# Kernel optimization log

Hardware: AMD Instinct MI355X
Metric: run time of the kernel (lower is better)

The kernel has to match this reference:

```python
import jax, jax.numpy as jnp
import numpy as np


def haar_level(x):
    """One 2D Haar (periodization-equivalent for even sizes) DWT on [B,K,C,H,W].
    Returns [B,4K,C,H/2,W/2] with per-parent band order (LL, Hx, Hy, Hxy),
    matching the tree's append order yl, yh0, yh1, yh2."""
    B, K, C, H, W = x.shape
    x = x.reshape(B, K, C, H // 2, 2, W // 2, 2)
    a = x[:, :, :, :, 0, :, 0]
    b = x[:, :, :, :, 0, :, 1]
    c = x[:, :, :, :, 1, :, 0]
    d = x[:, :, :, :, 1, :, 1]
    ll = (a + b + c + d) * 0.5
    h1 = (a - b + c - d) * 0.5   # high along width
    h2 = (a + b - c - d) * 0.5   # high along height
    h3 = (a - b - c + d) * 0.5   # diagonal
    out = jnp.stack([ll, h1, h2, h3], axis=2)  # [B,K,4,C,H/2,W/2]
    return out.reshape(B, 4 * K, C, H // 2, W // 2)


def conv2d(x, w, b, stride, pad):
    y = jax.lax.conv_general_dilated(
        x, w, window_strides=(stride, stride),
        padding=[(pad, pad), (pad, pad)],
        dimension_numbers=('NCHW', 'OIHW', 'NCHW'))
    return y + b[None, :, None, None]


def setup_inputs() -> dict:
    key = jax.random.key(0)
    ks = jax.random.split(key, 9)
    s = 0.05
    return {
        'x':        jax.random.normal(ks[0], (64, 3, 224, 224), dtype=jnp.float32),
        'w_s1':     jax.random.normal(ks[1], (192, 3, 7, 7), dtype=jnp.float32) * s,
        'b_s1':     jax.random.normal(ks[2], (192,), dtype=jnp.float32) * s,
        'w_s2':     jax.random.normal(ks[3], (192, 192, 7, 7), dtype=jnp.float32) * s,
        'b_s2':     jax.random.normal(ks[4], (192,), dtype=jnp.float32) * s,
        'w_p':      jax.random.normal(ks[5], (768, 960, 3, 3), dtype=jnp.float32) * s,
        'b_p':      jax.random.normal(ks[6], (768,), dtype=jnp.float32) * s,
        'cls_token': jax.random.normal(ks[7], (1, 1, 768), dtype=jnp.float32),
        'positions': jax.random.normal(ks[8], (50, 768), dtype=jnp.float32),
    }


def reference(x, w_s1, b_s1, w_s2, b_s2, w_p, b_p, cls_token, positions):
    B = x.shape[0]
    # ---- 4-level full Haar wavelet packet tree (vectorized over subbands) ----
    t = x[:, None]                      # [B,1,3,224,224]
    for _ in range(4):
        t = haar_level(t)               # -> [B,256,3,14,14]
    wav = t.reshape(B, 256 * 3, 14, 14)  # [B,768,14,14] (tree concat order)
    # ---- spatial branch: two strided 7x7 convs (224 -> 56 -> 14) ----
    sp = conv2d(x, w_s1, b_s1, stride=4, pad=3)
    sp = conv2d(sp, w_s2, b_s2, stride=4, pad=3)   # [B,192,14,14]
    feat = jnp.concatenate([wav, sp], axis=1)      # [B,960,14,14]
    # ---- patch projection conv 3x3 s2 -> 7x7, flatten to tokens ----
    y = conv2d(feat, w_p, b_p, stride=2, pad=1)    # [B,768,7,7]
    y = y.reshape(B, 768, 49).transpose(0, 2, 1)   # [B,49,768]
    cls = jnp.broadcast_to(cls_token, (B, 1, 768))
    y = jnp.concatenate([cls, y], axis=1) + positions  # [B,50,768]
    return y
```

## Files before the change

### kernel.cpp

```cpp
#include <hip/hip_runtime.h>
#include <stdint.h>

typedef __attribute__((ext_vector_type(8))) short short8;
typedef __attribute__((ext_vector_type(4))) float floatx4;

__device__ inline unsigned short f2bf(float f){
  union { float fv; unsigned int u; } v; v.fv = f;
  unsigned int u = v.u;
  unsigned int r = ((u >> 16) & 1u) + 0x7FFFu;
  return (unsigned short)((u + r) >> 16);
}

__device__ __forceinline__ void async16(const void* g, void* l){
  __builtin_amdgcn_global_load_lds(
      (const __attribute__((address_space(1))) unsigned int*)g,
      (__attribute__((address_space(3))) unsigned int*)l, 16, 0, 0);
}

#define PBAR(N) do {                                              \
    asm volatile("s_waitcnt vmcnt(" #N ")" ::: "memory");          \
    __builtin_amdgcn_s_barrier();                                  \
    asm volatile("" ::: "memory");                                 \
  } while (0)

__global__ void prep_w1(const float* __restrict__ w, unsigned short* __restrict__ w1p){
  int i = blockIdx.x*256 + threadIdx.x;
  if (i >= 192*192) return;
  int k = i % 192, o = i / 192;
  int cc = k >> 3, kx = k & 7;
  unsigned short v = 0;
  if (cc < 21 && kx < 7){
    int c = cc / 7, ky = cc % 7;
    v = f2bf(w[(o*3 + c)*49 + ky*7 + kx]);
  }
  w1p[i] = v;
}
__global__ void prep_w2(const float* __restrict__ w, unsigned short* __restrict__ w2p){
  int i = blockIdx.x*256 + threadIdx.x;
  if (i >= 192*9408) return;
  int k = i % 9408, o = i / 9408;
  int g = k / 192, c = k % 192;
  int ky = g / 7, kx = g % 7;
  w2p[i] = f2bf(w[((o*192 + c)*7 + ky)*7 + kx]);
}
__global__ void prep_w3(const float* __restrict__ w, unsigned short* __restrict__ w3p){
  int i = blockIdx.x*256 + threadIdx.x;
  if (i >= 768*8640) return;
  int k = i % 8640, o = i / 8640;
  int g = k / 960, c = k % 960;
  int ky = g / 3, kx = g % 3;
  w3p[i] = f2bf(w[((o*960 + c)*3 + ky)*3 + kx]);
}
__global__ void prep_zp(unsigned int* __restrict__ zp){
  zp[threadIdx.x] = 0u;
}
__global__ void zero_f32(float* __restrict__ p, int n){
  int i = blockIdx.x*256 + threadIdx.x;
  if (i < n) p[i] = 0.f;
}

__global__ void pad_x2(const float* __restrict__ x, unsigned short* __restrict__ xh2){
  int idx = blockIdx.x*256 + threadIdx.x;
  if (idx >= 64*3*230*56*8) return;
  int kx = idx & 7; int t = idx >> 3;
  int ox = t % 56;  t /= 56;
  int iy = t % 230; t /= 230;
  int row = iy - 3;
  int col = 4*ox - 3 + kx;
  unsigned short v = 0;
  if (row >= 0 && row < 224 && col >= 0 && col < 224)
    v = f2bf(x[((size_t)t*224 + row)*224 + col]);
  xh2[idx] = v;
}

__global__ void wavelet_kernel(const float* __restrict__ x, unsigned short* __restrict__ feat){
  int blk = blockIdx.x;
  int j = blk % 14; blk /= 14;
  int i = blk % 14; blk /= 14;
  int c = blk % 3;  int b = blk / 3;
  int t = threadIdx.x;
  int u = t >> 4, v = t & 15;
  float val = x[((size_t)(b*3 + c)*224 + (i*16 + u))*224 + (j*16 + v)];
  #pragma unroll
  for (int bit = 1; bit < 64; bit <<= 1){
    float p = __shfl_xor(val, bit);
    val = (t & bit) ? (p - val) : (val + p);
  }
  __shared__ float s[256];
  #pragma unroll
  for (int bit = 64; bit < 256; bit <<= 1){
    s[t] = val; __syncthreads();
    float p = s[t ^ bit]; __syncthreads();
    val = (t & bit) ? (p - val) : (val + p);
  }
  s[t] = val; __syncthreads();
  int k = t;
  int d1 = (k>>6)&3, d2 = (k>>4)&3, d3 = (k>>2)&3, d4 = k&3;
  int mr = (d1>>1) | ((d2>>1)<<1) | ((d3>>1)<<2) | ((d4>>1)<<3);
  int mc = (d1&1)  | ((d2&1)<<1)  | ((d3&1)<<2)  | ((d4&1)<<3);
  float outv = s[mr*16 + mc] * 0.0625f;
  feat[((size_t)((b*14 + i)*14 + j))*960 + (k*3 + c)] = f2bf(outv);
}

__global__ __launch_bounds__(256) void conv1_gemm(const unsigned short* __restrict__ xh2,
                                                  const unsigned short* __restrict__ w1p,
                                                  const float* __restrict__ b1,
                                                  unsigned short* __restrict__ sp1){
  __shared__ unsigned short As[2][128*64], Bs[2][64*64];
  int m0 = blockIdx.x*128, n0 = blockIdx.y*64;
  int tid = threadIdx.x, wave = tid >> 6, lane = tid & 63;
  int l16 = lane & 15, quad = lane >> 4;
  int wy = wave >> 1, wx = wave & 1;
  int r8 = lane >> 3, kb = (lane & 7) ^ r8;

  int Abase[4];
  #pragma unroll
  for (int j = 0; j < 4; j++){
    int row = wave*32 + j*8 + r8;
    int m = m0 + row;
    int ox = m % 56; int t = m / 56; int oy = t % 56; int b = t / 56;
    Abase[j] = (b*690 + 4*oy)*448 + ox*8;
  }
  const unsigned short* pB0 = w1p + (n0 + wave*16 + r8)*192 + kb*8;
  const unsigned short* pB1 = pB0 + 8*192;

  int sw = l16 & 7;
  int xo0 = ((quad    ) ^ sw)*8;
  int xo1 = ((quad + 4) ^ sw)*8;
  int aoff[4];
  #pragma unroll
  for (int mt = 0; mt < 4; mt++) aoff[mt] = (wy*64 + mt*16 + l16)*64;
  int boff0 = (wx*32 + l16)*64, boff1 = boff0 + 16*64;

  floatx4 acc[4][2];
  #pragma unroll
  for (int mt = 0; mt < 4; mt++)
    #pragma unroll
    for (int nt = 0; nt < 2; nt++) acc[mt][nt] = (floatx4){0.f,0.f,0.f,0.f};

  auto stage = [&](int i, int buf){
    int cc = i*8 + kb;
    int c = (cc*147) >> 10;
    int ky = cc - 7*c;
    int koff = (c*230 + ky)*448;
    #pragma unroll
    for (int j = 0; j < 4; j++)
      async16(xh2 + Abase[j] + koff, (void*)&As[buf][(wave*32 + j*8)*64]);
    async16(pB0 + i*64, (void*)&Bs[buf][(wave*16    )*64]);
    async16(pB1 + i*64, (void*)&Bs[buf][(wave*16 + 8)*64]);
  };

  stage(0, 0);
  __syncthreads();
  #pragma unroll
  for (int i = 0; i < 3; i++){
    int buf = i & 1;
    if (i < 2) stage(i+1, buf ^ 1);
    #pragma unroll
    for (int ks = 0; ks < 2; ks++){
      int xo = ks ? xo1 : xo0;
      short8 b0 = *(const short8*)&Bs[buf][boff0 + xo];
      short8 b1 = *(const short8*)&Bs[buf][boff1 + xo];
      #pragma unroll
      for (int mt = 0; mt < 4; mt++){
        short8 a = *(const short8*)&As[buf][aoff[mt] + xo];
        acc[mt][0] = __builtin_amdgcn_mfma_f32_16x16x32_bf16(a, b0, acc[mt][0], 0, 0, 0);
        acc[mt][1] = __builtin_amdgcn_mfma_f32_16x16x32_bf16(a, b1, acc[mt][1], 0, 0, 0);
      }
    }
    __syncthreads();
  }

  #pragma unroll
  for (int mt = 0; mt < 4; mt++){
    #pragma unroll
    for (int rg = 0; rg < 4; rg++){
      int row = wy*64 + mt*16 + quad*4 + rg;
      size_t ob = (size_t)(m0 + row)*192;
      #pragma unroll
      for (int nt = 0; nt < 2; nt++){
        int nn = n0 + wx*32 + nt*16 + l16;
        sp1[ob + nn] = f2bf(acc[mt][nt][rg] + b1[nn]);
      }
    }
  }
}

template<int MODE>
__global__ __launch_bounds__(256, 4) void conv_ks(const unsigned short* __restrict__ Ain,
                                                  const unsigned short* __restrict__ Bt,
                                                  const unsigned short* __restrict__ zp,
                                                  float* __restrict__ pout){
  constexpr int OH  = (MODE==2) ? 14 : 7;
  constexpr int OW  = OH;
  constexpr int IH  = (MODE==2) ? 56 : 14;
  constexpr int IW  = IH;
  constexpr int Cin = (MODE==2) ? 192 : 960;
  constexpr int KW  = (MODE==2) ? 7 : 3;
  constexpr int S   = (MODE==2) ? 4 : 2;
  constexpr int P   = (MODE==2) ? 3 : 1;
  constexpr int K   = (MODE==2) ? 9408 : 8640;
  constexpr int K2  = K/2;
  constexpr int NB  = K2/32;
  constexpr int MTI = (MODE==2) ? 98 : 25;
  constexpr int NTI = (MODE==2) ? 3 : 12;
  constexpr int GRP = 8*NTI;
  constexpr int PERSEG = (MODE==2) ? 13*GRP : 4*GRP;
  constexpr int M   = (MODE==2) ? 12544 : 3136;
  constexpr int NF  = (MODE==2) ? 192 : 768;

  int id = blockIdx.x;
  int kseg = id / PERSEG; int rem = id % PERSEG;
  int g = rem / GRP, r2 = rem % GRP;
  int mtile = g*8 + (r2 & 7);
  if (mtile >= MTI) return;
  int ntile = r2 >> 3;
  int m0 = mtile*128, n0 = ntile*64;

  __shared__ unsigned short As[3][4096], Bs[3][2048];

  int tid = threadIdx.x, wv = tid >> 6, lane = tid & 63;
  int l16 = lane & 15, quad = lane >> 4;
  int wy = wv >> 1, wx = wv & 1;

  int rl = lane >> 2;
  int go = ((lane & 3) ^ ((lane >> 3) & 3))*8;

  int iyb[2], ixb[2], abase[2];
  #pragma unroll
  for (int j = 0; j < 2; j++){
    int r = (wv + j*4)*16 + rl;
    int m = m0 + r; if (MODE == 3 && m > M-1) m = M-1;
    int ox = m % OW; int t = m / OW; int oy = t % OH; int bb = t / OH;
    iyb[j] = S*oy - P; ixb[j] = S*ox - P;
    abase[j] = ((bb*IH + iyb[j])*IW + ixb[j])*Cin + go;
  }
  const unsigned short* pB = Bt + (size_t)(n0 + wv*16 + rl)*K + kseg*K2 + go;

  int k0 = kseg*K2;
  int c0 = k0 % Cin;
  int gk = k0 / Cin;
  int ky = gk / KW, kx = gk % KW;
  int k0n = 0;

  int xo = (quad ^ ((l16 >> 1) & 3))*8;

  floatx4 acc[4][2];
  #pragma unroll
  for (int mt = 0; mt < 4; mt++)
    #pragma unroll
    for (int nt = 0; nt < 2; nt++) acc[mt][nt] = (floatx4){0.f,0.f,0.f,0.f};

  auto stage = [&](int buf){
    int koff = (ky*IW + kx)*Cin + c0;
    #pragma unroll
    for (int j = 0; j < 2; j++){
      int iy = iyb[j] + ky, ix = ixb[j] + kx;
      const unsigned short* pa = ((unsigned)iy < (unsigned)IH && (unsigned)ix < (unsigned)IW)
                                 ? (Ain + abase[j] + koff) : zp;
      async16(pa, (void*)&As[buf][(wv + j*4)*512]);
    }
    async16(pB + k0n, (void*)&Bs[buf][wv*512]);
    k0n += 32;
    c0 += 32;
    if (c0 == Cin){ c0 = 0; kx++; if (kx == KW){ kx = 0; ky++; } }
  };

  auto compute = [&](int buf){
    short8 b0 = *(const short8*)&Bs[buf][(wx*32      + l16)*32 + xo];
    short8 b1 = *(const short8*)&Bs[buf][(wx*32 + 16 + l16)*32 + xo];
    short8 a0 = *(const short8*)&As[buf][(wy*64       + l16)*32 + xo];
    short8 a1 = *(const short8*)&As[buf][(wy*64 + 16  + l16)*32 + xo];
    short8 a2 = *(const short8*)&As[buf][(wy*64 + 32  + l16)*32 + xo];
    short8 a3 = *(const short8*)&As[buf][(wy*64 + 48  + l16)*32 + xo];
    acc[0][0] = __builtin_amdgcn_mfma_f32_16x16x32_bf16(a0, b0, acc[0][0], 0, 0, 0);
    acc[0][1] = __builtin_amdgcn_mfma_f32_16x16x32_bf16(a0, b1, acc[0][1], 0, 0, 0);
    acc[1][0] = __builtin_amdgcn_mfma_f32_16x16x32_bf16(a1, b0, acc[1][0], 0, 0, 0);
    acc[1][1] = __builtin_amdgcn_mfma_f32_16x16x32_bf16(a1, b1, acc[1][1], 0, 0, 0);
    acc[2][0] = __builtin_amdgcn_mfma_f32_16x16x32_bf16(a2, b0, acc[2][0], 0, 0, 0);
    acc[2][1] = __builtin_amdgcn_mfma_f32_16x16x32_bf16(a2, b1, acc[2][1], 0, 0, 0);
    acc[3][0] = __builtin_amdgcn_mfma_f32_16x16x32_bf16(a3, b0, acc[3][0], 0, 0, 0);
    acc[3][1] = __builtin_amdgcn_mfma_f32_16x16x32_bf16(a3, b1, acc[3][1], 0, 0, 0);
  };

  stage(0); stage(1);
  int bc = 0;
  for (int i = 0; i < NB - 2; i++){
    PBAR(3);
    int bn = bc + 2; if (bn >= 3) bn -= 3;
    stage(bn);
    compute(bc);
    bc = (bc == 2) ? 0 : bc + 1;
  }
  PBAR(3);
  compute(bc);
  bc = (bc == 2) ? 0 : bc + 1;
  PBAR(0);
  compute(bc);

  #pragma unroll
  for (int mt = 0; mt < 4; mt++){
    #pragma unroll
    for (int rg = 0; rg < 4; rg++){
      int row = wy*64 + mt*16 + quad*4 + rg;
      int mm = m0 + row;
      if (MODE == 3 && mm >= M) continue;
      #pragma unroll
      for (int nt = 0; nt < 2; nt++){
        int nn = n0 + wx*32 + nt*16 + l16;
        atomicAdd(&pout[(size_t)mm*NF + nn], acc[mt][nt][rg]);
      }
    }
  }
}

__global__ void comb2(const float* __restrict__ pc, const float* __restrict__ bias,
                      unsigned short* __restrict__ feat){
  int i = blockIdx.x*256 + threadIdx.x;
  int n = i % 192, m = i / 192;
  feat[(size_t)m*960 + 768 + n] = f2bf(pc[i] + bias[n]);
}
__global__ void comb3(const float* __restrict__ pc, const float* __restrict__ bias,
                      const float* __restrict__ pos, float* __restrict__ out){
  int i = blockIdx.x*256 + threadIdx.x;
  int n = i % 768, m = i / 768;
  int b2 = m / 49, tt = m - b2*49;
  float v = pc[(size_t)m*768 + n] + bias[n] + pos[(size_t)(1 + tt)*768 + n];
  out[((size_t)(m + b2 + 1))*768 + n] = v;
}

__global__ void cls_kernel(const float* __restrict__ cls, const float* __restrict__ pos,
                           float* __restrict__ out){
  int i = blockIdx.x*256 + threadIdx.x;
  if (i >= 64*768) return;
  int e = i % 768, b = i / 768;
  out[(size_t)(b*50)*768 + e] = cls[e] + pos[e];
}

extern "C" void kernel_launch(void* const* d_in, const int* in_sizes, int n_in,
                              void* d_out, int out_size, void* d_ws, size_t ws_size,
                              hipStream_t stream){
  (void)in_sizes; (void)n_in; (void)out_size;
  const float* x    = (const float*)d_in[0];
  const float* w_s1 = (const float*)d_in[1];
  const float* b_s1 = (const float*)d_in[2];
  const float* w_s2 = (const float*)d_in[3];
  const float* b_s2 = (const float*)d_in[4];
  const float* w_p  = (const float*)d_in[5];
  const float* b_p  = (const float*)d_in[6];
  const float* cls  = (const float*)d_in[7];
  const float* pos  = (const float*)d_in[8];
  float* out = (float*)d_out;

  char* ws = (char*)d_ws;
  if (ws_size < 118235136u) return;
  unsigned short* w1p  = (unsigned short*)(ws + 0);
  unsigned short* sp1  = (unsigned short*)(ws + 131072);
  unsigned short* zp   = (unsigned short*)(ws + 77201408u);
  unsigned short* w2p  = (unsigned short*)(ws + 77266944u);
  unsigned short* w3p  = (unsigned short*)(ws + 80879616u);
  unsigned short* feat = (unsigned short*)(ws + 94150656u);
  unsigned short* xh2  = (unsigned short*)(ws + 77266944u);
  float* pc2 = (float*)(ws + 80879616u);
  float* pc3 = (float*)(ws + 131072);

  prep_w1<<<(192*192 + 255)/256, 256, 0, stream>>>(w_s1, w1p);
  pad_x2<<<(64*3*230*56*8)/256, 256, 0, stream>>>(x, xh2);
  conv1_gemm<<<dim3(1568, 3), 256, 0, stream>>>(xh2, w1p, b_s1, sp1);
  prep_w2<<<(192*9408 + 255)/256, 256, 0, stream>>>(w_s2, w2p);
  prep_zp<<<1, 64, 0, stream>>>((unsigned int*)zp);
  wavelet_kernel<<<64*3*14*14, 256, 0, stream>>>(x, feat);

  zero_f32<<<9408, 256, 0, stream>>>(pc2, 12544*192);
  conv_ks<2><<<624, 256, 0, stream>>>(sp1, w2p, zp, pc2);
  comb2<<<9408, 256, 0, stream>>>(pc2, b_s2, feat);

  prep_w3<<<(768*8640 + 255)/256, 256, 0, stream>>>(w_p, w3p);
  zero_f32<<<9600, 256, 0, stream>>>(pc3, 3200*768);
  conv_ks<3><<<768, 256, 0, stream>>>(feat, w3p, zp, pc3);
  comb3<<<9408, 256, 0, stream>>>(pc3, b_p, pos, out);
  cls_kernel<<<(64*768 + 255)/256, 256, 0, stream>>>(cls, pos, out);
}
```

Baseline: 457.3 us.

## Split conv K-reduction into four segments and vectorize padded input staging

The split-K factor of both implicit-GEMM convolutions goes from 2 to 4, with segment bounds computed in 32-wide K blocks, and the grid sizes are doubled to match. The aim is to give the GPU more blocks, since 624 or 768 blocks leave it underfilled. The cost is more atomic or partial-sum traffic into the fp32 accumulators. Separately, the input padding kernel now has each thread build 8 bf16 values and write them with one 16-byte store, instead of one thread per element.

```diff
diff --git a/kernel.cpp b/kernel.cpp
--- a/kernel.cpp
+++ b/kernel.cpp
@@ -59,18 +59,22 @@
   if (i < n) p[i] = 0.f;
 }
 
-__global__ void pad_x2(const float* __restrict__ x, unsigned short* __restrict__ xh2){
+__global__ void pad_x8(const float* __restrict__ x, unsigned short* __restrict__ xh2){
   int idx = blockIdx.x*256 + threadIdx.x;
-  if (idx >= 64*3*230*56*8) return;
-  int kx = idx & 7; int t = idx >> 3;
-  int ox = t % 56;  t /= 56;
-  int iy = t % 230; t /= 230;
+  int ox = idx % 56; int t = idx / 56;
+  int iy = t % 230;  t /= 230;
   int row = iy - 3;
-  int col = 4*ox - 3 + kx;
-  unsigned short v = 0;
-  if (row >= 0 && row < 224 && col >= 0 && col < 224)
-    v = f2bf(x[((size_t)t*224 + row)*224 + col]);
-  xh2[idx] = v;
+  short8 o = (short8){0,0,0,0,0,0,0,0};
+  if ((unsigned)row < 224u){
+    const float* src = x + ((size_t)t*224 + row)*224;
+    int cbase = 4*ox - 3;
+    #pragma unroll
+    for (int kx = 0; kx < 8; kx++){
+      int col = cbase + kx;
+      if ((unsigned)col < 224u) o[kx] = (short)f2bf(src[col]);
+    }
+  }
+  *(short8*)(xh2 + (size_t)idx*8) = o;
 }
 
 __global__ void wavelet_kernel(const float* __restrict__ x, unsigned short* __restrict__ feat){
@@ -200,8 +204,8 @@
   constexpr int S   = (MODE==2) ? 4 : 2;
   constexpr int P   = (MODE==2) ? 3 : 1;
   constexpr int K   = (MODE==2) ? 9408 : 8640;
-  constexpr int K2  = K/2;
-  constexpr int NB  = K2/32;
+  constexpr int NBODY = K/32;
+  constexpr int KSEG  = 4;
   constexpr int MTI = (MODE==2) ? 98 : 25;
   constexpr int NTI = (MODE==2) ? 3 : 12;
   constexpr int GRP = 8*NTI;
@@ -217,6 +221,10 @@
   int ntile = r2 >> 3;
   int m0 = mtile*128, n0 = ntile*64;
 
+  int bs = (NBODY*kseg)/KSEG, be = (NBODY*(kseg+1))/KSEG;
+  int NB = be - bs;
+  int k0 = bs*32;
+
   __shared__ unsigned short As[3][4096], Bs[3][2048];
 
   int tid = threadIdx.x, wv = tid >> 6, lane = tid & 63;
@@ -235,9 +243,8 @@
     iyb[j] = S*oy - P; ixb[j] = S*ox - P;
     abase[j] = ((bb*IH + iyb[j])*IW + ixb[j])*Cin + go;
   }
-  const unsigned short* pB = Bt + (size_t)(n0 + wv*16 + rl)*K + kseg*K2 + go;
-
-  int k0 = kseg*K2;
+  const unsigned short* pB = Bt + (size_t)(n0 + wv*16 + rl)*K + k0 + go;
+
   int c0 = k0 % Cin;
   int gk = k0 / Cin;
   int ky = gk / KW, kx = gk % KW;
@@ -365,19 +372,19 @@
   float* pc3 = (float*)(ws + 131072);
 
   prep_w1<<<(192*192 + 255)/256, 256, 0, stream>>>(w_s1, w1p);
-  pad_x2<<<(64*3*230*56*8)/256, 256, 0, stream>>>(x, xh2);
+  pad_x8<<<64*3*230*56/256, 256, 0, stream>>>(x, xh2);
   conv1_gemm<<<dim3(1568, 3), 256, 0, stream>>>(xh2, w1p, b_s1, sp1);
   prep_w2<<<(192*9408 + 255)/256, 256, 0, stream>>>(w_s2, w2p);
   prep_zp<<<1, 64, 0, stream>>>((unsigned int*)zp);
   wavelet_kernel<<<64*3*14*14, 256, 0, stream>>>(x, feat);
 
   zero_f32<<<9408, 256, 0, stream>>>(pc2, 12544*192);
-  conv_ks<2><<<624, 256, 0, stream>>>(sp1, w2p, zp, pc2);
+  conv_ks<2><<<1248, 256, 0, stream>>>(sp1, w2p, zp, pc2);
   comb2<<<9408, 256, 0, stream>>>(pc2, b_s2, feat);
 
   prep_w3<<<(768*8640 + 255)/256, 256, 0, stream>>>(w_p, w3p);
   zero_f32<<<9600, 256, 0, stream>>>(pc3, 3200*768);
-  conv_ks<3><<<768, 256, 0, stream>>>(feat, w3p, zp, pc3);
+  conv_ks<3><<<1536, 256, 0, stream>>>(feat, w3p, zp, pc3);
   comb3<<<9408, 256, 0, stream>>>(pc3, b_p, pos, out);
   cls_kernel<<<(64*768 + 255)/256, 256, 0, stream>>>(cls, pos, out);
 }
```

After: 482.8 us. 5.6% more time.
